# Kernel tuning notes

Hardware: AMD Instinct MI355X
Metric: run time of the kernel (lower is better)

The kernel has to match this reference:

```python
import jax, jax.numpy as jnp
import numpy as np

B, T = 64, 2048
DEC, ENC, ATT, LOC, K = 1024, 512, 128, 32, 31


def setup_inputs() -> dict:
    key = jax.random.key(0)
    ks = jax.random.split(key, 9)
    inv = lambda n: 1.0 / np.sqrt(n)
    return {
        "query": jax.random.normal(ks[0], (B, DEC), dtype=jnp.float32),
        "values": jax.random.normal(ks[1], (B, T, ENC), dtype=jnp.float32),
        "cumulative_attention_weights": jax.random.uniform(ks[2], (B, T), dtype=jnp.float32),
        "mask": jnp.zeros((B, T), dtype=bool),
        "Q_w": jax.random.uniform(ks[3], (ATT, DEC), jnp.float32, -inv(DEC), inv(DEC)),
        "Q_b": jax.random.uniform(ks[4], (ATT,), jnp.float32, -inv(DEC), inv(DEC)),
        "V_w": jax.random.uniform(ks[5], (ATT, ENC), jnp.float32, -inv(ENC), inv(ENC)),
        "conv_w": jax.random.uniform(ks[6], (LOC, 1, K), jnp.float32, -inv(K), inv(K)),
        "loc_proj_w": jax.random.uniform(ks[7], (ATT, LOC), jnp.float32, -inv(LOC), inv(LOC)),
        "v_w": jax.random.uniform(ks[8], (1, ATT), jnp.float32, -inv(ATT), inv(ATT)),
    }


def reference(query, values, cumulative_attention_weights, mask,
              Q_w, Q_b, V_w, conv_w, loc_proj_w, v_w):
    # query projection: [B, 1, ATT] (broadcast over T)
    q = query @ Q_w.T + Q_b                       # [B, ATT]
    q = q[:, None, :]
    # values cache: [B, T, ATT]
    v_cache = jnp.einsum("bte,ae->bta", values, V_w)
    # location features: Conv1d(1 -> LOC, k=31, same padding) over cum weights
    x = cumulative_attention_weights[:, None, :]   # [B, 1, T]
    loc = jax.lax.conv_general_dilated(
        x, conv_w, window_strides=(1,), padding="SAME",
        dimension_numbers=("NCH", "OIH", "NCH"))   # [B, LOC, T]
    loc = jnp.einsum("bct,ac->bta", loc, loc_proj_w)  # [B, T, ATT]
    # additive attention energies
    energies = jnp.tanh(q + v_cache + loc) @ v_w[0]   # [B, T]
    energies = jnp.where(mask, -jnp.inf, energies)
    attention_weights = jax.nn.softmax(energies, axis=1)
    # context: [B, ENC]
    attention_context = jnp.einsum("bt,bte->be", attention_weights, values)
    return attention_context, attention_weights
```

## Files before the change

kernel.cpp:

```cpp
#include <hip/hip_runtime.h>
#include <hip/hip_bf16.h>
#include <math.h>

#define B_  64
#define T_  2048
#define DEC_ 1024
#define ENC_ 512
#define ATT_ 128
#define LOC_ 32
#define KW_  31

typedef __attribute__((ext_vector_type(8))) short short8;
typedef __attribute__((ext_vector_type(4))) float f32x4;
typedef __attribute__((ext_vector_type(4))) unsigned int u32x4;

__device__ inline unsigned short bf16_rn(float x) {
    unsigned int u = __builtin_bit_cast(unsigned int, x);
    unsigned int r = u + 0x7fffu + ((u >> 16) & 1u);
    return (unsigned short)(r >> 16);
}
__device__ inline float bf16_to_f(unsigned short h) {
    unsigned int u = ((unsigned int)h) << 16;
    return __builtin_bit_cast(float, u);
}

__device__ inline void cvt_split8_exact(const float* f, short8& hi8, short8& lo8) {
    u32x4 hw, lw;
    #pragma unroll
    for (int p = 0; p < 4; ++p) {
        float a = f[2 * p], b2 = f[2 * p + 1];
        unsigned u0 = __builtin_bit_cast(unsigned, a);
        unsigned u1 = __builtin_bit_cast(unsigned, b2);
        unsigned r0 = u0 + 0x7fffu + ((u0 >> 16) & 1u);
        unsigned r1 = u1 + 0x7fffu + ((u1 >> 16) & 1u);
        hw[p] = (r0 >> 16) | (r1 & 0xffff0000u);
        float d0 = a  - __builtin_bit_cast(float, r0 & 0xffff0000u);
        float d1 = b2 - __builtin_bit_cast(float, r1 & 0xffff0000u);
        unsigned v0 = __builtin_bit_cast(unsigned, d0);
        unsigned v1 = __builtin_bit_cast(unsigned, d1);
        unsigned s0 = v0 + 0x7fffu + ((v0 >> 16) & 1u);
        unsigned s1 = v1 + 0x7fffu + ((v1 >> 16) & 1u);
        lw[p] = (s0 >> 16) | (s1 & 0xffff0000u);
    }
    hi8 = __builtin_bit_cast(short8, hw);
    lo8 = __builtin_bit_cast(short8, lw);
}

__global__ __launch_bounds__(256) void prep_kernel(
    const float* __restrict__ query, const float* __restrict__ Q_w,
    const float* __restrict__ Q_b, const float* __restrict__ conv_w,
    const float* __restrict__ loc_proj_w, const float* __restrict__ V_w,
    float* __restrict__ qbuf,
    unsigned short* __restrict__ Bph, unsigned short* __restrict__ Bpl,
    unsigned short* __restrict__ effh, unsigned short* __restrict__ effl)
{
    int bi = blockIdx.x, tid = threadIdx.x;
    if (bi < 256) {
        int b = bi >> 2, grp = bi & 3;
        __shared__ float sq[DEC_];
        *(float4*)(&sq[tid * 4]) = *(const float4*)(query + (size_t)b * DEC_ + tid * 4);
        __syncthreads();
        int w = tid >> 6, lane = tid & 63;
        int a0 = grp * 32 + w * 8;
        for (int p = 0; p < 4; ++p) {
            int a = a0 + 2 * p;
            const float* r0 = Q_w + (size_t)a * DEC_;
            const float* r1 = r0 + DEC_;
            float s0 = 0.f, s1 = 0.f;
            #pragma unroll
            for (int i = 0; i < 4; ++i) {
                float4 q0 = *(const float4*)(r0 + i * 256 + lane * 4);
                float4 q1 = *(const float4*)(r1 + i * 256 + lane * 4);
                float4 xq = *(const float4*)(sq + i * 256 + lane * 4);
                s0 += q0.x * xq.x + q0.y * xq.y + q0.z * xq.z + q0.w * xq.w;
                s1 += q1.x * xq.x + q1.y * xq.y + q1.z * xq.z + q1.w * xq.w;
            }
            #pragma unroll
            for (int m = 32; m >= 1; m >>= 1) {
                s0 += __shfl_xor(s0, m, 64);
                s1 += __shfl_xor(s1, m, 64);
            }
            if (lane == 0) {
                qbuf[b * ATT_ + a]     = s0 + Q_b[a];
                qbuf[b * ATT_ + a + 1] = s1 + Q_b[a + 1];
            }
        }
    } else if (bi == 256) {
        __shared__ float slp[ATT_ * LOC_];
        __shared__ float scw[LOC_ * KW_];
        for (int i = tid; i < ATT_ * LOC_; i += 256) slp[i] = loc_proj_w[i];
        for (int i = tid; i < LOC_ * KW_; i += 256) scw[i] = conv_w[i];
        __syncthreads();
        if (tid < ATT_) {
            int n = tid;
            for (int k = 0; k < 32; ++k) {
                float s = 0.f;
                if (k < KW_)
                    #pragma unroll
                    for (int c = 0; c < LOC_; ++c)
                        s += slp[n * LOC_ + c] * scw[c * KW_ + k];
                unsigned short h = bf16_rn(s);
                effh[n * 32 + k] = h;
                effl[n * 32 + k] = bf16_rn(s - bf16_to_f(h));
            }
        }
    } else {
        int g0 = (bi - 257) * 512;
        #pragma unroll
        for (int p = 0; p < 2; ++p) {
            int gi = g0 + p * 256 + tid;
            int n  = gi >> 7;
            int kq = (gi & 127) * 4;
            float4 v = ((const float4*)V_w)[gi];
            ushort4 h4, l4;
            h4.x = bf16_rn(v.x); l4.x = bf16_rn(v.x - bf16_to_f(h4.x));
            h4.y = bf16_rn(v.y); l4.y = bf16_rn(v.y - bf16_to_f(h4.y));
            h4.z = bf16_rn(v.z); l4.z = bf16_rn(v.z - bf16_to_f(h4.z));
            h4.w = bf16_rn(v.w); l4.w = bf16_rn(v.w - bf16_to_f(h4.w));
            int dst = (kq >> 5) * 4096 + n * 32 + (kq & 31);
            *(ushort4*)(Bph + dst) = h4;
            *(ushort4*)(Bpl + dst) = l4;
        }
    }
}

__global__ __launch_bounds__(256, 2) void energy_ctx_kernel(
    const float* __restrict__ values, const float* __restrict__ cum,
    const float* __restrict__ qbuf,
    const unsigned short* __restrict__ Bph, const unsigned short* __restrict__ Bpl,
    const unsigned short* __restrict__ effh, const unsigned short* __restrict__ effl,
    const float* __restrict__ vw, const unsigned char* __restrict__ mask,
    float* __restrict__ wU, float* __restrict__ bstats,
    float* __restrict__ ctxpart)
{
    __shared__ float sx[160];
    __shared__ float se[128];
    __shared__ float red[512];

    const int tid = threadIdx.x;
    const int bx  = blockIdx.x;
    const int b   = bx >> 4;
    const int t0  = (bx & 15) * 128;

    if (tid < 160) {
        int g = t0 - 15 + tid;
        sx[tid] = (g >= 0 && g < T_) ? cum[b * T_ + g] : 0.f;
    }
    __syncthreads();

    const int w      = tid >> 6;
    const int lane   = tid & 63;
    const int lane15 = lane & 15;
    const int quad   = lane >> 4;

    f32x4 acc[2][8];
    #pragma unroll
    for (int i = 0; i < 2; ++i)
        #pragma unroll
        for (int j = 0; j < 8; ++j) acc[i][j] = (f32x4){0.f, 0.f, 0.f, 0.f};

    const float* abase = values + ((size_t)b * T_ + t0 + w * 32 + lane15) * ENC_ + quad * 8;
    const unsigned short* bbh = Bph + lane15 * 32 + quad * 8;
    const unsigned short* bbl = Bpl + lane15 * 32 + quad * 8;

    float4 pfA[2][2], pfB[2][2];
    #pragma unroll
    for (int i = 0; i < 2; ++i) {
        pfA[i][0] = *(const float4*)(abase + i * 16 * ENC_);
        pfA[i][1] = *(const float4*)(abase + i * 16 * ENC_ + 4);
        pfB[i][0] = *(const float4*)(abase + i * 16 * ENC_ + 32);
        pfB[i][1] = *(const float4*)(abase + i * 16 * ENC_ + 36);
    }

    auto halfstep = [&](float4 (&pfX)[2][2], int kc, bool pre) {
        short8 ah[2], al[2];
        #pragma unroll
        for (int i = 0; i < 2; ++i) {
            float fb[8] = {pfX[i][0].x, pfX[i][0].y, pfX[i][0].z, pfX[i][0].w,
                           pfX[i][1].x, pfX[i][1].y, pfX[i][1].z, pfX[i][1].w};
            cvt_split8_exact(fb, ah[i], al[i]);
        }
        short8 bh[8], bl[8];
        const unsigned short* bb_h = bbh + (kc >> 5) * 4096;
        const unsigned short* bb_l = bbl + (kc >> 5) * 4096;
        #pragma unroll
        for (int j = 0; j < 8; ++j) {
            bh[j] = *(const short8*)(bb_h + j * 512);
            bl[j] = *(const short8*)(bb_l + j * 512);
        }
        __builtin_amdgcn_sched_barrier(0);
        if (pre) {
            #pragma unroll
            for (int i = 0; i < 2; ++i) {
                pfX[i][0] = *(const float4*)(abase + i * 16 * ENC_ + kc + 64);
                pfX[i][1] = *(const float4*)(abase + i * 16 * ENC_ + kc + 68);
            }
        }
        __builtin_amdgcn_sched_barrier(0);
        #pragma unroll
        for (int j = 0; j < 8; ++j)
            #pragma unroll
            for (int i = 0; i < 2; ++i) {
                acc[i][j] = __builtin_amdgcn_mfma_f32_16x16x32_bf16(ah[i], bh[j], acc[i][j], 0, 0, 0);
                acc[i][j] = __builtin_amdgcn_mfma_f32_16x16x32_bf16(ah[i], bl[j], acc[i][j], 0, 0, 0);
                acc[i][j] = __builtin_amdgcn_mfma_f32_16x16x32_bf16(al[i], bh[j], acc[i][j], 0, 0, 0);
            }
    };

    for (int kc = 0; kc < ENC_; kc += 64) {
        halfstep(pfA, kc,      kc + 64 < ENC_);
        halfstep(pfB, kc + 32, kc + 96 < ENC_);
    }

    {
        short8 ah[2], al[2];
        #pragma unroll
        for (int i = 0; i < 2; ++i) {
            int base = w * 32 + i * 16 + lane15 + quad * 8;
            float xv[8];
            #pragma unroll
            for (int j2 = 0; j2 < 8; ++j2) xv[j2] = sx[base + j2];
            cvt_split8_exact(xv, ah[i], al[i]);
        }
        #pragma unroll
        for (int j = 0; j < 8; ++j) {
            int n = j * 16 + lane15;
            short8 bh = *(const short8*)(effh + n * 32 + quad * 8);
            short8 bl = *(const short8*)(effl + n * 32 + quad * 8);
            #pragma unroll
            for (int i = 0; i < 2; ++i) {
                acc[i][j] = __builtin_amdgcn_mfma_f32_16x16x32_bf16(ah[i], bh, acc[i][j], 0, 0, 0);
                acc[i][j] = __builtin_amdgcn_mfma_f32_16x16x32_bf16(ah[i], bl, acc[i][j], 0, 0, 0);
                acc[i][j] = __builtin_amdgcn_mfma_f32_16x16x32_bf16(al[i], bh, acc[i][j], 0, 0, 0);
            }
        }
    }

    float qv[8], vv[8];
    #pragma unroll
    for (int j = 0; j < 8; ++j) {
        int n = j * 16 + lane15;
        qv[j] = qbuf[b * ATT_ + n];
        vv[j] = vw[n];
    }
    #pragma unroll
    for (int i = 0; i < 2; ++i)
        #pragma unroll
        for (int r = 0; r < 4; ++r) {
            float s = 0.f;
            #pragma unroll
            for (int j = 0; j < 8; ++j)
                s += vv[j] * tanhf(acc[i][j][r] + qv[j]);
            #pragma unroll
            for (int m = 8; m >= 1; m >>= 1) s += __shfl_xor(s, m, 64);
            if (lane15 == 0)
                se[w * 32 + i * 16 + quad * 4 + r] = s;
        }
    __syncthreads();

    if (tid < 128 && mask[b * T_ + t0 + tid]) se[tid] = -INFINITY;
    __syncthreads();

    float e0 = se[lane * 2], e1 = se[lane * 2 + 1];
    float mx = fmaxf(e0, e1);
    #pragma unroll
    for (int m = 32; m >= 1; m >>= 1) mx = fmaxf(mx, __shfl_xor(mx, m, 64));
    float w0 = 0.f, w1 = 0.f;
    if (mx > -INFINITY) {
        w0 = expf(e0 - mx);
        w1 = expf(e1 - mx);
    }
    float sm = w0 + w1;
    #pragma unroll
    for (int m = 32; m >= 1; m >>= 1) sm += __shfl_xor(sm, m, 64);
    __syncthreads();

    if (w == 0) {
        se[lane * 2]     = w0;
        se[lane * 2 + 1] = w1;
        *(float2*)(wU + b * T_ + t0 + lane * 2) = make_float2(w0, w1);
        if (lane == 0)
            *(float2*)(bstats + bx * 2) = make_float2(mx, sm);
    }
    __syncthreads();

    {
        int tt = tid >> 7;
        int e4 = (tid & 127) * 4;
        const float* vp = values + ((size_t)b * T_ + t0 + tt * 64) * ENC_ + e4;
        float4 cacc = make_float4(0.f, 0.f, 0.f, 0.f);
        #pragma unroll 8
        for (int t = 0; t < 64; ++t) {
            float4 v = *(const float4*)(vp + (size_t)t * ENC_);
            float wv = se[tt * 64 + t];
            cacc.x += wv * v.x; cacc.y += wv * v.y;
            cacc.z += wv * v.z; cacc.w += wv * v.w;
        }
        if (tt == 1) *(float4*)&red[e4] = cacc;
        __syncthreads();
        if (tt == 0) {
            float4 o = *(const float4*)&red[e4];
            float4 tot = make_float4(cacc.x + o.x, cacc.y + o.y,
                                     cacc.z + o.z, cacc.w + o.w);
            *(float4*)(ctxpart + (size_t)bx * ENC_ + e4) = tot;
        }
    }
}

__global__ __launch_bounds__(256) void combine_kernel(
    const float* __restrict__ bstats, const float* __restrict__ ctxpart,
    const float* __restrict__ wU, float* __restrict__ out)
{
    int b = blockIdx.x, tid = threadIdx.x;
    __shared__ float smx[16], ssm[16], ssc[16];
    if (tid < 16) {
        float2 st = *(const float2*)(bstats + (b * 16 + tid) * 2);
        smx[tid] = st.x; ssm[tid] = st.y;
    }
    __syncthreads();
    float M = -INFINITY;
    #pragma unroll
    for (int k = 0; k < 16; ++k) M = fmaxf(M, smx[k]);
    if (tid < 16)
        ssc[tid] = (smx[tid] > -INFINITY) ? expf(smx[tid] - M) : 0.f;
    __syncthreads();
    float S = 0.f;
    #pragma unroll
    for (int k = 0; k < 16; ++k) S += ssm[k] * ssc[k];
    float invS = 1.f / S;

    float* ctx  = out;
    float* wout = out + B_ * ENC_;

    float cx = 0.f, cy = 0.f;
    #pragma unroll
    for (int k = 0; k < 16; ++k) {
        float2 v = *(const float2*)(ctxpart + (size_t)(b * 16 + k) * ENC_ + tid * 2);
        cx += v.x * ssc[k]; cy += v.y * ssc[k];
    }
    *(float2*)(ctx + b * ENC_ + tid * 2) = make_float2(cx * invS, cy * invS);

    #pragma unroll
    for (int p = 0; p < 8; ++p) {
        int t = p * 256 + tid;
        wout[b * T_ + t] = wU[b * T_ + t] * ssc[t >> 7] * invS;
    }
}

extern "C" void kernel_launch(void* const* d_in, const int* in_sizes, int n_in,
                              void* d_out, int out_size, void* d_ws, size_t ws_size,
                              hipStream_t stream) {
    const float* query        = (const float*)d_in[0];
    const float* values       = (const float*)d_in[1];
    const float* cum          = (const float*)d_in[2];
    const unsigned char* mask = (const unsigned char*)d_in[3];
    const float* Q_w          = (const float*)d_in[4];
    const float* Q_b          = (const float*)d_in[5];
    const float* V_w          = (const float*)d_in[6];
    const float* conv_w       = (const float*)d_in[7];
    const float* loc_proj_w   = (const float*)d_in[8];
    const float* v_w          = (const float*)d_in[9];

    float* out = (float*)d_out;
    char*  ws  = (char*)d_ws;
    float*          qbuf     = (float*)(ws);
    unsigned short* Bph      = (unsigned short*)(ws + 32768);
    unsigned short* Bpl      = (unsigned short*)(ws + 163840);
    unsigned short* effh     = (unsigned short*)(ws + 294912);
    unsigned short* effl     = (unsigned short*)(ws + 303104);
    float*          wU       = (float*)(ws + 311296);
    float*          bstats   = (float*)(ws + 835584);
    float*          ctxpart  = (float*)(ws + 843776);

    prep_kernel<<<289, 256, 0, stream>>>(query, Q_w, Q_b, conv_w, loc_proj_w, V_w,
                                         qbuf, Bph, Bpl, effh, effl);
    energy_ctx_kernel<<<1024, 256, 0, stream>>>(values, cum, qbuf, Bph, Bpl,
                                                effh, effl, v_w, mask,
                                                wU, bstats, ctxpart);
    combine_kernel<<<B_, 256, 0, stream>>>(bstats, ctxpart, wU, out);
}
```

Before: 469.1 us.

## Stage packed V_w bf16 tiles into LDS via async global-to-LDS double buffering

Packs the hi/lo bf16 split of V_w into one interleaved buffer laid out per 32-wide K chunk. The energy kernel now double-buffers each chunk into shared memory with global_load_lds and block barriers, instead of every wave loading the B fragments directly from global or L2. The A-side prefetch drops from two halves to one chunk ahead. This adds 32KB of LDS per block, which may limit occupancy, and adds a barrier per K chunk.

```diff
diff --git a/kernel.cpp b/kernel.cpp
--- a/kernel.cpp
+++ b/kernel.cpp
@@ -50,8 +50,7 @@
     const float* __restrict__ query, const float* __restrict__ Q_w,
     const float* __restrict__ Q_b, const float* __restrict__ conv_w,
     const float* __restrict__ loc_proj_w, const float* __restrict__ V_w,
-    float* __restrict__ qbuf,
-    unsigned short* __restrict__ Bph, unsigned short* __restrict__ Bpl,
+    float* __restrict__ qbuf, unsigned short* __restrict__ Bpk,
     unsigned short* __restrict__ effh, unsigned short* __restrict__ effl)
 {
     int bi = blockIdx.x, tid = threadIdx.x;
@@ -117,22 +116,27 @@
             h4.y = bf16_rn(v.y); l4.y = bf16_rn(v.y - bf16_to_f(h4.y));
             h4.z = bf16_rn(v.z); l4.z = bf16_rn(v.z - bf16_to_f(h4.z));
             h4.w = bf16_rn(v.w); l4.w = bf16_rn(v.w - bf16_to_f(h4.w));
-            int dst = (kq >> 5) * 4096 + n * 32 + (kq & 31);
-            *(ushort4*)(Bph + dst) = h4;
-            *(ushort4*)(Bpl + dst) = l4;
+            int c = kq >> 5;
+            int j = n >> 7 == 0 ? (n >> 4) : (n >> 4);
+            int l = ((kq & 31) >> 3) * 16 + (n & 15);
+            int e = kq & 7;
+            int dst = c * 8192 + (n >> 4) * 512 + l * 8 + e;
+            (void)j;
+            *(ushort4*)(Bpk + dst)        = h4;
+            *(ushort4*)(Bpk + dst + 4096) = l4;
         }
     }
 }
 
 __global__ __launch_bounds__(256, 2) void energy_ctx_kernel(
     const float* __restrict__ values, const float* __restrict__ cum,
-    const float* __restrict__ qbuf,
-    const unsigned short* __restrict__ Bph, const unsigned short* __restrict__ Bpl,
+    const float* __restrict__ qbuf, const unsigned short* __restrict__ Bpk,
     const unsigned short* __restrict__ effh, const unsigned short* __restrict__ effl,
     const float* __restrict__ vw, const unsigned char* __restrict__ mask,
     float* __restrict__ wU, float* __restrict__ bstats,
     float* __restrict__ ctxpart)
 {
+    __shared__ unsigned short sB[2][8192];
     __shared__ float sx[160];
     __shared__ float se[128];
     __shared__ float red[512];
@@ -160,56 +164,71 @@
         for (int j = 0; j < 8; ++j) acc[i][j] = (f32x4){0.f, 0.f, 0.f, 0.f};
 
     const float* abase = values + ((size_t)b * T_ + t0 + w * 32 + lane15) * ENC_ + quad * 8;
-    const unsigned short* bbh = Bph + lane15 * 32 + quad * 8;
-    const unsigned short* bbl = Bpl + lane15 * 32 + quad * 8;
-
-    float4 pfA[2][2], pfB[2][2];
+
+    auto stageB = [&](int buf, int c) {
+        const unsigned short* src = Bpk + c * 8192 + w * 512 + lane * 8;
+        #pragma unroll
+        for (int r = 0; r < 4; ++r) {
+            __builtin_amdgcn_global_load_lds(
+                (const __attribute__((address_space(1))) unsigned int*)(src + r * 2048),
+                (__attribute__((address_space(3))) unsigned int*)(&sB[buf][r * 2048 + w * 512]),
+                16, 0, 0);
+        }
+    };
+
+    float4 pf[2][2];
+    stageB(0, 0);
+    __builtin_amdgcn_sched_barrier(0);
     #pragma unroll
     for (int i = 0; i < 2; ++i) {
-        pfA[i][0] = *(const float4*)(abase + i * 16 * ENC_);
-        pfA[i][1] = *(const float4*)(abase + i * 16 * ENC_ + 4);
-        pfB[i][0] = *(const float4*)(abase + i * 16 * ENC_ + 32);
-        pfB[i][1] = *(const float4*)(abase + i * 16 * ENC_ + 36);
-    }
-
-    auto halfstep = [&](float4 (&pfX)[2][2], int kc, bool pre) {
+        pf[i][0] = *(const float4*)(abase + i * 16 * ENC_);
+        pf[i][1] = *(const float4*)(abase + i * 16 * ENC_ + 4);
+    }
+    __builtin_amdgcn_sched_barrier(0);
+    asm volatile("s_waitcnt vmcnt(4)");
+    __builtin_amdgcn_sched_barrier(0);
+    __builtin_amdgcn_s_barrier();
+
+    int cur = 0;
+    for (int c = 0; c < 16; ++c) {
+        if (c + 1 < 16) stageB(cur ^ 1, c + 1);
+        __builtin_amdgcn_sched_barrier(0);
+
         short8 ah[2], al[2];
         #pragma unroll
         for (int i = 0; i < 2; ++i) {
-            float fb[8] = {pfX[i][0].x, pfX[i][0].y, pfX[i][0].z, pfX[i][0].w,
-                           pfX[i][1].x, pfX[i][1].y, pfX[i][1].z, pfX[i][1].w};
+            float fb[8] = {pf[i][0].x, pf[i][0].y, pf[i][0].z, pf[i][0].w,
+                           pf[i][1].x, pf[i][1].y, pf[i][1].z, pf[i][1].w};
             cvt_split8_exact(fb, ah[i], al[i]);
         }
-        short8 bh[8], bl[8];
-        const unsigned short* bb_h = bbh + (kc >> 5) * 4096;
-        const unsigned short* bb_l = bbl + (kc >> 5) * 4096;
+        if (c + 1 < 16) {
+            int kc = (c + 1) * 32;
+            #pragma unroll
+            for (int i = 0; i < 2; ++i) {
+                pf[i][0] = *(const float4*)(abase + i * 16 * ENC_ + kc);
+                pf[i][1] = *(const float4*)(abase + i * 16 * ENC_ + kc + 4);
+            }
+        }
+
         #pragma unroll
         for (int j = 0; j < 8; ++j) {
-            bh[j] = *(const short8*)(bb_h + j * 512);
-            bl[j] = *(const short8*)(bb_l + j * 512);
-        }
-        __builtin_amdgcn_sched_barrier(0);
-        if (pre) {
+            short8 bh = *(const short8*)&sB[cur][j * 512 + lane * 8];
+            short8 bl = *(const short8*)&sB[cur][4096 + j * 512 + lane * 8];
             #pragma unroll
             for (int i = 0; i < 2; ++i) {
-                pfX[i][0] = *(const float4*)(abase + i * 16 * ENC_ + kc + 64);
-                pfX[i][1] = *(const float4*)(abase + i * 16 * ENC_ + kc + 68);
-            }
-        }
-        __builtin_amdgcn_sched_barrier(0);
-        #pragma unroll
-        for (int j = 0; j < 8; ++j)
-            #pragma unroll
-            for (int i = 0; i < 2; ++i) {
-                acc[i][j] = __builtin_amdgcn_mfma_f32_16x16x32_bf16(ah[i], bh[j], acc[i][j], 0, 0, 0);
-                acc[i][j] = __builtin_amdgcn_mfma_f32_16x16x32_bf16(ah[i], bl[j], acc[i][j], 0, 0, 0);
-                acc[i][j] = __builtin_amdgcn_mfma_f32_16x16x32_bf16(al[i], bh[j], acc[i][j], 0, 0, 0);
-            }
-    };
-
-    for (int kc = 0; kc < ENC_; kc += 64) {
-        halfstep(pfA, kc,      kc + 64 < ENC_);
-        halfstep(pfB, kc + 32, kc + 96 < ENC_);
+                acc[i][j] = __builtin_amdgcn_mfma_f32_16x16x32_bf16(ah[i], bh, acc[i][j], 0, 0, 0);
+                acc[i][j] = __builtin_amdgcn_mfma_f32_16x16x32_bf16(ah[i], bl, acc[i][j], 0, 0, 0);
+                acc[i][j] = __builtin_amdgcn_mfma_f32_16x16x32_bf16(al[i], bh, acc[i][j], 0, 0, 0);
+            }
+        }
+
+        if (c + 1 < 16) {
+            __builtin_amdgcn_sched_barrier(0);
+            asm volatile("s_waitcnt vmcnt(4)");
+            __builtin_amdgcn_sched_barrier(0);
+            __builtin_amdgcn_s_barrier();
+            cur ^= 1;
+        }
     }
 
     {
@@ -364,8 +383,7 @@
     float* out = (float*)d_out;
     char*  ws  = (char*)d_ws;
     float*          qbuf     = (float*)(ws);
-    unsigned short* Bph      = (unsigned short*)(ws + 32768);
-    unsigned short* Bpl      = (unsigned short*)(ws + 163840);
+    unsigned short* Bpk      = (unsigned short*)(ws + 32768);
     unsigned short* effh     = (unsigned short*)(ws + 294912);
     unsigned short* effl     = (unsigned short*)(ws + 303104);
     float*          wU       = (float*)(ws + 311296);
@@ -373,8 +391,8 @@
     float*          ctxpart  = (float*)(ws + 843776);
 
     prep_kernel<<<289, 256, 0, stream>>>(query, Q_w, Q_b, conv_w, loc_proj_w, V_w,
-                                         qbuf, Bph, Bpl, effh, effl);
-    energy_ctx_kernel<<<1024, 256, 0, stream>>>(values, cum, qbuf, Bph, Bpl,
+                                         qbuf, Bpk, effh, effl);
+    energy_ctx_kernel<<<1024, 256, 0, stream>>>(values, cum, qbuf, Bpk,
                                                 effh, effl, v_w, mask,
                                                 wU, bstats, ctxpart);
     combine_kernel<<<B_, 256, 0, stream>>>(bstats, ctxpart, wU, out);
```

Result: no change. 460.3 us (-1.9%).

## Make energy/context work wave-local with 128-thread blocks and per-wave softmax partials

Applied to the files above, without the earlier changes.

Shrinks the energy kernel to 128-thread blocks of two independent waves. Each wave computes its own 32-timestep softmax partial and context partial, so block-wide barriers and the cross-wave shared reduction go away. The A-operand prefetch is simplified from two ping-pong buffers to one. The cost is four times as many partials (64 per batch) for the combine kernel to merge, and less prefetch depth to hide load latency.

```diff
diff --git a/kernel.cpp b/kernel.cpp
--- a/kernel.cpp
+++ b/kernel.cpp
@@ -124,7 +124,7 @@
     }
 }
 
-__global__ __launch_bounds__(256, 2) void energy_ctx_kernel(
+__global__ __launch_bounds__(128, 4) void energy_ctx_kernel(
     const float* __restrict__ values, const float* __restrict__ cum,
     const float* __restrict__ qbuf,
     const unsigned short* __restrict__ Bph, const unsigned short* __restrict__ Bpl,
@@ -133,67 +133,68 @@
     float* __restrict__ wU, float* __restrict__ bstats,
     float* __restrict__ ctxpart)
 {
-    __shared__ float sx[160];
-    __shared__ float se[128];
-    __shared__ float red[512];
-
-    const int tid = threadIdx.x;
-    const int bx  = blockIdx.x;
-    const int b   = bx >> 4;
-    const int t0  = (bx & 15) * 128;
-
-    if (tid < 160) {
-        int g = t0 - 15 + tid;
-        sx[tid] = (g >= 0 && g < T_) ? cum[b * T_ + g] : 0.f;
-    }
-    __syncthreads();
-
-    const int w      = tid >> 6;
-    const int lane   = tid & 63;
+    __shared__ float sxw[2][80];
+    __shared__ float sew[2][32];
+
+    const int tid  = threadIdx.x;
+    const int bx   = blockIdx.x;
+    const int b    = bx >> 5;
+    const int sub  = bx & 31;
+    const int w    = tid >> 6;
+    const int lane = tid & 63;
+    const int t0w  = sub * 64 + w * 32;
+    const int cid  = sub * 2 + w;
+
     const int lane15 = lane & 15;
     const int quad   = lane >> 4;
 
+    {
+        int g = t0w - 15 + lane;
+        sxw[w][lane] = (g >= 0 && g < T_) ? cum[b * T_ + g] : 0.f;
+        if (lane < 16) {
+            int g2 = t0w + 49 + lane;
+            sxw[w][64 + lane] = (g2 >= 0 && g2 < T_) ? cum[b * T_ + g2] : 0.f;
+        }
+    }
+
     f32x4 acc[2][8];
     #pragma unroll
     for (int i = 0; i < 2; ++i)
         #pragma unroll
         for (int j = 0; j < 8; ++j) acc[i][j] = (f32x4){0.f, 0.f, 0.f, 0.f};
 
-    const float* abase = values + ((size_t)b * T_ + t0 + w * 32 + lane15) * ENC_ + quad * 8;
+    const float* abase = values + ((size_t)b * T_ + t0w + lane15) * ENC_ + quad * 8;
     const unsigned short* bbh = Bph + lane15 * 32 + quad * 8;
     const unsigned short* bbl = Bpl + lane15 * 32 + quad * 8;
 
-    float4 pfA[2][2], pfB[2][2];
+    float4 pf[2][2];
     #pragma unroll
     for (int i = 0; i < 2; ++i) {
-        pfA[i][0] = *(const float4*)(abase + i * 16 * ENC_);
-        pfA[i][1] = *(const float4*)(abase + i * 16 * ENC_ + 4);
-        pfB[i][0] = *(const float4*)(abase + i * 16 * ENC_ + 32);
-        pfB[i][1] = *(const float4*)(abase + i * 16 * ENC_ + 36);
-    }
-
-    auto halfstep = [&](float4 (&pfX)[2][2], int kc, bool pre) {
+        pf[i][0] = *(const float4*)(abase + i * 16 * ENC_);
+        pf[i][1] = *(const float4*)(abase + i * 16 * ENC_ + 4);
+    }
+
+    for (int kc = 0; kc < ENC_; kc += 32) {
         short8 ah[2], al[2];
         #pragma unroll
         for (int i = 0; i < 2; ++i) {
-            float fb[8] = {pfX[i][0].x, pfX[i][0].y, pfX[i][0].z, pfX[i][0].w,
-                           pfX[i][1].x, pfX[i][1].y, pfX[i][1].z, pfX[i][1].w};
+            float fb[8] = {pf[i][0].x, pf[i][0].y, pf[i][0].z, pf[i][0].w,
+                           pf[i][1].x, pf[i][1].y, pf[i][1].z, pf[i][1].w};
             cvt_split8_exact(fb, ah[i], al[i]);
         }
         short8 bh[8], bl[8];
-        const unsigned short* bb_h = bbh + (kc >> 5) * 4096;
-        const unsigned short* bb_l = bbl + (kc >> 5) * 4096;
+        const int chunk = (kc >> 5) * 4096;
         #pragma unroll
         for (int j = 0; j < 8; ++j) {
-            bh[j] = *(const short8*)(bb_h + j * 512);
-            bl[j] = *(const short8*)(bb_l + j * 512);
+            bh[j] = *(const short8*)(bbh + chunk + j * 512);
+            bl[j] = *(const short8*)(bbl + chunk + j * 512);
         }
         __builtin_amdgcn_sched_barrier(0);
-        if (pre) {
+        if (kc + 32 < ENC_) {
             #pragma unroll
             for (int i = 0; i < 2; ++i) {
-                pfX[i][0] = *(const float4*)(abase + i * 16 * ENC_ + kc + 64);
-                pfX[i][1] = *(const float4*)(abase + i * 16 * ENC_ + kc + 68);
+                pf[i][0] = *(const float4*)(abase + i * 16 * ENC_ + kc + 32);
+                pf[i][1] = *(const float4*)(abase + i * 16 * ENC_ + kc + 36);
             }
         }
         __builtin_amdgcn_sched_barrier(0);
@@ -205,21 +206,16 @@
                 acc[i][j] = __builtin_amdgcn_mfma_f32_16x16x32_bf16(ah[i], bl[j], acc[i][j], 0, 0, 0);
                 acc[i][j] = __builtin_amdgcn_mfma_f32_16x16x32_bf16(al[i], bh[j], acc[i][j], 0, 0, 0);
             }
-    };
-
-    for (int kc = 0; kc < ENC_; kc += 64) {
-        halfstep(pfA, kc,      kc + 64 < ENC_);
-        halfstep(pfB, kc + 32, kc + 96 < ENC_);
     }
 
     {
         short8 ah[2], al[2];
         #pragma unroll
         for (int i = 0; i < 2; ++i) {
-            int base = w * 32 + i * 16 + lane15 + quad * 8;
+            int base = i * 16 + lane15 + quad * 8;
             float xv[8];
             #pragma unroll
-            for (int j2 = 0; j2 < 8; ++j2) xv[j2] = sx[base + j2];
+            for (int j2 = 0; j2 < 8; ++j2) xv[j2] = sxw[w][base + j2];
             cvt_split8_exact(xv, ah[i], al[i]);
         }
         #pragma unroll
@@ -254,56 +250,45 @@
             #pragma unroll
             for (int m = 8; m >= 1; m >>= 1) s += __shfl_xor(s, m, 64);
             if (lane15 == 0)
-                se[w * 32 + i * 16 + quad * 4 + r] = s;
-        }
-    __syncthreads();
-
-    if (tid < 128 && mask[b * T_ + t0 + tid]) se[tid] = -INFINITY;
-    __syncthreads();
-
-    float e0 = se[lane * 2], e1 = se[lane * 2 + 1];
-    float mx = fmaxf(e0, e1);
+                sew[w][i * 16 + quad * 4 + r] = s;
+        }
+
+    float e = (lane < 32) ? sew[w][lane] : -INFINITY;
+    if (lane < 32 && mask[b * T_ + t0w + lane]) e = -INFINITY;
+    float mx = e;
     #pragma unroll
     for (int m = 32; m >= 1; m >>= 1) mx = fmaxf(mx, __shfl_xor(mx, m, 64));
-    float w0 = 0.f, w1 = 0.f;
-    if (mx > -INFINITY) {
-        w0 = expf(e0 - mx);
-        w1 = expf(e1 - mx);
-    }
-    float sm = w0 + w1;
+    float w0 = 0.f;
+    if (mx > -INFINITY && lane < 32) w0 = expf(e - mx);
+    float sm = w0;
     #pragma unroll
     for (int m = 32; m >= 1; m >>= 1) sm += __shfl_xor(sm, m, 64);
-    __syncthreads();
-
-    if (w == 0) {
-        se[lane * 2]     = w0;
-        se[lane * 2 + 1] = w1;
-        *(float2*)(wU + b * T_ + t0 + lane * 2) = make_float2(w0, w1);
-        if (lane == 0)
-            *(float2*)(bstats + bx * 2) = make_float2(mx, sm);
-    }
-    __syncthreads();
+
+    if (lane < 32) {
+        sew[w][lane] = w0;
+        wU[b * T_ + t0w + lane] = w0;
+    }
+    if (lane == 0)
+        *(float2*)(bstats + (b * 64 + cid) * 2) = make_float2(mx, sm);
 
     {
-        int tt = tid >> 7;
-        int e4 = (tid & 127) * 4;
-        const float* vp = values + ((size_t)b * T_ + t0 + tt * 64) * ENC_ + e4;
-        float4 cacc = make_float4(0.f, 0.f, 0.f, 0.f);
+        int e8 = lane * 8;
+        const float* vp = values + ((size_t)b * T_ + t0w) * ENC_ + e8;
+        float4 c0 = make_float4(0.f, 0.f, 0.f, 0.f);
+        float4 c1 = make_float4(0.f, 0.f, 0.f, 0.f);
         #pragma unroll 8
-        for (int t = 0; t < 64; ++t) {
-            float4 v = *(const float4*)(vp + (size_t)t * ENC_);
-            float wv = se[tt * 64 + t];
-            cacc.x += wv * v.x; cacc.y += wv * v.y;
-            cacc.z += wv * v.z; cacc.w += wv * v.w;
-        }
-        if (tt == 1) *(float4*)&red[e4] = cacc;
-        __syncthreads();
-        if (tt == 0) {
-            float4 o = *(const float4*)&red[e4];
-            float4 tot = make_float4(cacc.x + o.x, cacc.y + o.y,
-                                     cacc.z + o.z, cacc.w + o.w);
-            *(float4*)(ctxpart + (size_t)bx * ENC_ + e4) = tot;
-        }
+        for (int t = 0; t < 32; ++t) {
+            float4 v0 = *(const float4*)(vp + (size_t)t * ENC_);
+            float4 v1 = *(const float4*)(vp + (size_t)t * ENC_ + 4);
+            float wv = sew[w][t];
+            c0.x += wv * v0.x; c0.y += wv * v0.y;
+            c0.z += wv * v0.z; c0.w += wv * v0.w;
+            c1.x += wv * v1.x; c1.y += wv * v1.y;
+            c1.z += wv * v1.z; c1.w += wv * v1.w;
+        }
+        float* cp = ctxpart + (size_t)(b * 64 + cid) * ENC_ + e8;
+        *(float4*)(cp)     = c0;
+        *(float4*)(cp + 4) = c1;
     }
 }
 
@@ -312,30 +297,30 @@
     const float* __restrict__ wU, float* __restrict__ out)
 {
     int b = blockIdx.x, tid = threadIdx.x;
-    __shared__ float smx[16], ssm[16], ssc[16];
-    if (tid < 16) {
-        float2 st = *(const float2*)(bstats + (b * 16 + tid) * 2);
+    __shared__ float smx[64], ssm[64], ssc[64];
+    if (tid < 64) {
+        float2 st = *(const float2*)(bstats + (b * 64 + tid) * 2);
         smx[tid] = st.x; ssm[tid] = st.y;
     }
     __syncthreads();
     float M = -INFINITY;
     #pragma unroll
-    for (int k = 0; k < 16; ++k) M = fmaxf(M, smx[k]);
-    if (tid < 16)
+    for (int k = 0; k < 64; ++k) M = fmaxf(M, smx[k]);
+    if (tid < 64)
         ssc[tid] = (smx[tid] > -INFINITY) ? expf(smx[tid] - M) : 0.f;
     __syncthreads();
     float S = 0.f;
     #pragma unroll
-    for (int k = 0; k < 16; ++k) S += ssm[k] * ssc[k];
+    for (int k = 0; k < 64; ++k) S += ssm[k] * ssc[k];
     float invS = 1.f / S;
 
     float* ctx  = out;
     float* wout = out + B_ * ENC_;
 
     float cx = 0.f, cy = 0.f;
-    #pragma unroll
-    for (int k = 0; k < 16; ++k) {
-        float2 v = *(const float2*)(ctxpart + (size_t)(b * 16 + k) * ENC_ + tid * 2);
+    #pragma unroll 8
+    for (int k = 0; k < 64; ++k) {
+        float2 v = *(const float2*)(ctxpart + (size_t)(b * 64 + k) * ENC_ + tid * 2);
         cx += v.x * ssc[k]; cy += v.y * ssc[k];
     }
     *(float2*)(ctx + b * ENC_ + tid * 2) = make_float2(cx * invS, cy * invS);
@@ -343,7 +328,7 @@
     #pragma unroll
     for (int p = 0; p < 8; ++p) {
         int t = p * 256 + tid;
-        wout[b * T_ + t] = wU[b * T_ + t] * ssc[t >> 7] * invS;
+        wout[b * T_ + t] = wU[b * T_ + t] * ssc[t >> 5] * invS;
     }
 }
 
@@ -370,11 +355,11 @@
     unsigned short* effl     = (unsigned short*)(ws + 303104);
     float*          wU       = (float*)(ws + 311296);
     float*          bstats   = (float*)(ws + 835584);
-    float*          ctxpart  = (float*)(ws + 843776);
+    float*          ctxpart  = (float*)(ws + 868352);
 
     prep_kernel<<<289, 256, 0, stream>>>(query, Q_w, Q_b, conv_w, loc_proj_w, V_w,
                                          qbuf, Bph, Bpl, effh, effl);
-    energy_ctx_kernel<<<1024, 256, 0, stream>>>(values, cum, qbuf, Bph, Bpl,
+    energy_ctx_kernel<<<2048, 128, 0, stream>>>(values, cum, qbuf, Bph, Bpl,
                                                 effh, effl, v_w, mask,
                                                 wU, bstats, ctxpart);
     combine_kernel<<<B_, 256, 0, stream>>>(bstats, ctxpart, wU, out);
```

Result: slower. 770.5 us (+64.3%).

## Split energy GEMM over 8 waves with LDS-staged bf16 split of values

Applied to the files above, without the earlier changes.

Raises the energy/context block to 512 threads and arranges the 8 waves as a 4x2 grid over rows and attention columns. Each wave converts one 16x32 slab of values to hi/lo bf16 once and stages it in double-buffered LDS, with a barrier per K-chunk. The partial energies from the two column halves are summed through shared memory. The intent is more waves per CU and less register pressure to hide global-load latency, at the cost of per-chunk block barriers and extra LDS traffic.

```diff
diff --git a/kernel.cpp b/kernel.cpp
--- a/kernel.cpp
+++ b/kernel.cpp
@@ -23,7 +23,6 @@
     unsigned int u = ((unsigned int)h) << 16;
     return __builtin_bit_cast(float, u);
 }
-
 __device__ inline void cvt_split8_exact(const float* f, short8& hi8, short8& lo8) {
     u32x4 hw, lw;
     #pragma unroll
@@ -124,7 +123,7 @@
     }
 }
 
-__global__ __launch_bounds__(256, 2) void energy_ctx_kernel(
+__global__ __launch_bounds__(512, 4) void energy_ctx_kernel(
     const float* __restrict__ values, const float* __restrict__ cum,
     const float* __restrict__ qbuf,
     const unsigned short* __restrict__ Bph, const unsigned short* __restrict__ Bpl,
@@ -133,7 +132,10 @@
     float* __restrict__ wU, float* __restrict__ bstats,
     float* __restrict__ ctxpart)
 {
+    __shared__ unsigned short sAh[2][4096];
+    __shared__ unsigned short sAl[2][4096];
     __shared__ float sx[160];
+    __shared__ float sep[2][128];
     __shared__ float se[128];
     __shared__ float red[512];
 
@@ -146,85 +148,108 @@
         int g = t0 - 15 + tid;
         sx[tid] = (g >= 0 && g < T_) ? cum[b * T_ + g] : 0.f;
     }
-    __syncthreads();
 
     const int w      = tid >> 6;
     const int lane   = tid & 63;
     const int lane15 = lane & 15;
     const int quad   = lane >> 4;
-
-    f32x4 acc[2][8];
+    const int wr     = w >> 1;
+    const int wc     = w & 1;
+
+    f32x4 acc[2][4];
     #pragma unroll
     for (int i = 0; i < 2; ++i)
         #pragma unroll
-        for (int j = 0; j < 8; ++j) acc[i][j] = (f32x4){0.f, 0.f, 0.f, 0.f};
-
-    const float* abase = values + ((size_t)b * T_ + t0 + w * 32 + lane15) * ENC_ + quad * 8;
-    const unsigned short* bbh = Bph + lane15 * 32 + quad * 8;
-    const unsigned short* bbl = Bpl + lane15 * 32 + quad * 8;
-
-    float4 pfA[2][2], pfB[2][2];
-    #pragma unroll
-    for (int i = 0; i < 2; ++i) {
-        pfA[i][0] = *(const float4*)(abase + i * 16 * ENC_);
-        pfA[i][1] = *(const float4*)(abase + i * 16 * ENC_ + 4);
-        pfB[i][0] = *(const float4*)(abase + i * 16 * ENC_ + 32);
-        pfB[i][1] = *(const float4*)(abase + i * 16 * ENC_ + 36);
-    }
-
-    auto halfstep = [&](float4 (&pfX)[2][2], int kc, bool pre) {
+        for (int j = 0; j < 4; ++j) acc[i][j] = (f32x4){0.f, 0.f, 0.f, 0.f};
+
+    const float* wsrc = values + ((size_t)b * T_ + t0 + w * 16 + lane15) * ENC_ + quad * 8;
+    const unsigned short* bbh = Bph + wc * 2048 + lane15 * 32 + quad * 8;
+    const unsigned short* bbl = Bpl + wc * 2048 + lane15 * 32 + quad * 8;
+
+    float4 pA[2][2];
+    pA[0][0] = *(const float4*)(wsrc);
+    pA[0][1] = *(const float4*)(wsrc + 4);
+    pA[1][0] = *(const float4*)(wsrc + 32);
+    pA[1][1] = *(const float4*)(wsrc + 36);
+
+    {
+        float fb[8] = {pA[0][0].x, pA[0][0].y, pA[0][0].z, pA[0][0].w,
+                       pA[0][1].x, pA[0][1].y, pA[0][1].z, pA[0][1].w};
+        short8 h8, l8;
+        cvt_split8_exact(fb, h8, l8);
+        *(short8*)&sAh[0][(w * 64 + lane) * 8] = h8;
+        *(short8*)&sAl[0][(w * 64 + lane) * 8] = l8;
+    }
+    __syncthreads();
+
+    #pragma unroll
+    for (int c = 0; c < 16; ++c) {
+        const int cur = c & 1;
+        if (c + 2 < 16) {
+            pA[cur][0] = *(const float4*)(wsrc + (c + 2) * 32);
+            pA[cur][1] = *(const float4*)(wsrc + (c + 2) * 32 + 4);
+        }
+        __builtin_amdgcn_sched_barrier(0);
+
         short8 ah[2], al[2];
         #pragma unroll
         for (int i = 0; i < 2; ++i) {
-            float fb[8] = {pfX[i][0].x, pfX[i][0].y, pfX[i][0].z, pfX[i][0].w,
-                           pfX[i][1].x, pfX[i][1].y, pfX[i][1].z, pfX[i][1].w};
-            cvt_split8_exact(fb, ah[i], al[i]);
-        }
-        short8 bh[8], bl[8];
-        const unsigned short* bb_h = bbh + (kc >> 5) * 4096;
-        const unsigned short* bb_l = bbl + (kc >> 5) * 4096;
-        #pragma unroll
-        for (int j = 0; j < 8; ++j) {
-            bh[j] = *(const short8*)(bb_h + j * 512);
-            bl[j] = *(const short8*)(bb_l + j * 512);
-        }
-        __builtin_amdgcn_sched_barrier(0);
-        if (pre) {
-            #pragma unroll
-            for (int i = 0; i < 2; ++i) {
-                pfX[i][0] = *(const float4*)(abase + i * 16 * ENC_ + kc + 64);
-                pfX[i][1] = *(const float4*)(abase + i * 16 * ENC_ + kc + 68);
-            }
-        }
-        __builtin_amdgcn_sched_barrier(0);
-        #pragma unroll
-        for (int j = 0; j < 8; ++j)
-            #pragma unroll
-            for (int i = 0; i < 2; ++i) {
-                acc[i][j] = __builtin_amdgcn_mfma_f32_16x16x32_bf16(ah[i], bh[j], acc[i][j], 0, 0, 0);
-                acc[i][j] = __builtin_amdgcn_mfma_f32_16x16x32_bf16(ah[i], bl[j], acc[i][j], 0, 0, 0);
-                acc[i][j] = __builtin_amdgcn_mfma_f32_16x16x32_bf16(al[i], bh[j], acc[i][j], 0, 0, 0);
-            }
-    };
-
-    for (int kc = 0; kc < ENC_; kc += 64) {
-        halfstep(pfA, kc,      kc + 64 < ENC_);
-        halfstep(pfB, kc + 32, kc + 96 < ENC_);
+            ah[i] = *(const short8*)&sAh[cur][((wr * 2 + i) * 64 + lane) * 8];
+            al[i] = *(const short8*)&sAl[cur][((wr * 2 + i) * 64 + lane) * 8];
+        }
+
+        if (c + 1 < 16) {
+            float fb[8] = {pA[cur ^ 1][0].x, pA[cur ^ 1][0].y,
+                           pA[cur ^ 1][0].z, pA[cur ^ 1][0].w,
+                           pA[cur ^ 1][1].x, pA[cur ^ 1][1].y,
+                           pA[cur ^ 1][1].z, pA[cur ^ 1][1].w};
+            short8 h8, l8;
+            cvt_split8_exact(fb, h8, l8);
+            *(short8*)&sAh[cur ^ 1][(w * 64 + lane) * 8] = h8;
+            *(short8*)&sAl[cur ^ 1][(w * 64 + lane) * 8] = l8;
+        }
+
+        const int chunk = (c >> 0) * 0 + (c * 0);
+        const int coff  = (c) * 4096;
+        #pragma unroll
+        for (int jp = 0; jp < 2; ++jp) {
+            short8 bh[2], bl[2];
+            #pragma unroll
+            for (int u = 0; u < 2; ++u) {
+                bh[u] = *(const short8*)(bbh + coff + (jp * 2 + u) * 512);
+                bl[u] = *(const short8*)(bbl + coff + (jp * 2 + u) * 512);
+            }
+            #pragma unroll
+            for (int u = 0; u < 2; ++u)
+                #pragma unroll
+                for (int i = 0; i < 2; ++i) {
+                    acc[i][jp * 2 + u] = __builtin_amdgcn_mfma_f32_16x16x32_bf16(ah[i], bh[u], acc[i][jp * 2 + u], 0, 0, 0);
+                    acc[i][jp * 2 + u] = __builtin_amdgcn_mfma_f32_16x16x32_bf16(ah[i], bl[u], acc[i][jp * 2 + u], 0, 0, 0);
+                    acc[i][jp * 2 + u] = __builtin_amdgcn_mfma_f32_16x16x32_bf16(al[i], bh[u], acc[i][jp * 2 + u], 0, 0, 0);
+                }
+        }
+
+        if (c + 1 < 16) {
+            __builtin_amdgcn_sched_barrier(0);
+            asm volatile("s_waitcnt lgkmcnt(0)" ::: "memory");
+            __builtin_amdgcn_s_barrier();
+        }
+        (void)chunk;
     }
 
     {
         short8 ah[2], al[2];
         #pragma unroll
         for (int i = 0; i < 2; ++i) {
-            int base = w * 32 + i * 16 + lane15 + quad * 8;
+            int base = wr * 32 + i * 16 + lane15 + quad * 8;
             float xv[8];
             #pragma unroll
             for (int j2 = 0; j2 < 8; ++j2) xv[j2] = sx[base + j2];
             cvt_split8_exact(xv, ah[i], al[i]);
         }
         #pragma unroll
-        for (int j = 0; j < 8; ++j) {
-            int n = j * 16 + lane15;
+        for (int j = 0; j < 4; ++j) {
+            int n = wc * 64 + j * 16 + lane15;
             short8 bh = *(const short8*)(effh + n * 32 + quad * 8);
             short8 bl = *(const short8*)(effl + n * 32 + quad * 8);
             #pragma unroll
@@ -236,10 +261,10 @@
         }
     }
 
-    float qv[8], vv[8];
-    #pragma unroll
-    for (int j = 0; j < 8; ++j) {
-        int n = j * 16 + lane15;
+    float qv[4], vv[4];
+    #pragma unroll
+    for (int j = 0; j < 4; ++j) {
+        int n = wc * 64 + j * 16 + lane15;
         qv[j] = qbuf[b * ATT_ + n];
         vv[j] = vw[n];
     }
@@ -249,16 +274,20 @@
         for (int r = 0; r < 4; ++r) {
             float s = 0.f;
             #pragma unroll
-            for (int j = 0; j < 8; ++j)
+            for (int j = 0; j < 4; ++j)
                 s += vv[j] * tanhf(acc[i][j][r] + qv[j]);
             #pragma unroll
             for (int m = 8; m >= 1; m >>= 1) s += __shfl_xor(s, m, 64);
             if (lane15 == 0)
-                se[w * 32 + i * 16 + quad * 4 + r] = s;
-        }
-    __syncthreads();
-
-    if (tid < 128 && mask[b * T_ + t0 + tid]) se[tid] = -INFINITY;
+                sep[wc][wr * 32 + i * 16 + quad * 4 + r] = s;
+        }
+    __syncthreads();
+
+    if (tid < 128) {
+        float ee = sep[0][tid] + sep[1][tid];
+        if (mask[b * T_ + t0 + tid]) ee = -INFINITY;
+        se[tid] = ee;
+    }
     __syncthreads();
 
     float e0 = se[lane * 2], e1 = se[lane * 2 + 1];
@@ -285,24 +314,22 @@
     __syncthreads();
 
     {
-        int tt = tid >> 7;
-        int e4 = (tid & 127) * 4;
-        const float* vp = values + ((size_t)b * T_ + t0 + tt * 64) * ENC_ + e4;
-        float4 cacc = make_float4(0.f, 0.f, 0.f, 0.f);
+        int tt = tid >> 8;
+        int e2 = (tid & 255) * 2;
+        const float* vp = values + ((size_t)b * T_ + t0 + tt * 64) * ENC_ + e2;
+        float cx = 0.f, cy = 0.f;
         #pragma unroll 8
         for (int t = 0; t < 64; ++t) {
-            float4 v = *(const float4*)(vp + (size_t)t * ENC_);
+            float2 v = *(const float2*)(vp + (size_t)t * ENC_);
             float wv = se[tt * 64 + t];
-            cacc.x += wv * v.x; cacc.y += wv * v.y;
-            cacc.z += wv * v.z; cacc.w += wv * v.w;
-        }
-        if (tt == 1) *(float4*)&red[e4] = cacc;
+            cx += wv * v.x; cy += wv * v.y;
+        }
+        if (tt == 1) *(float2*)&red[e2] = make_float2(cx, cy);
         __syncthreads();
         if (tt == 0) {
-            float4 o = *(const float4*)&red[e4];
-            float4 tot = make_float4(cacc.x + o.x, cacc.y + o.y,
-                                     cacc.z + o.z, cacc.w + o.w);
-            *(float4*)(ctxpart + (size_t)bx * ENC_ + e4) = tot;
+            float2 o = *(const float2*)&red[e2];
+            *(float2*)(ctxpart + (size_t)bx * ENC_ + e2) =
+                make_float2(cx + o.x, cy + o.y);
         }
     }
 }
@@ -374,7 +401,7 @@
 
     prep_kernel<<<289, 256, 0, stream>>>(query, Q_w, Q_b, conv_w, loc_proj_w, V_w,
                                          qbuf, Bph, Bpl, effh, effl);
-    energy_ctx_kernel<<<1024, 256, 0, stream>>>(values, cum, qbuf, Bph, Bpl,
+    energy_ctx_kernel<<<1024, 512, 0, stream>>>(values, cum, qbuf, Bph, Bpl,
                                                 effh, effl, v_w, mask,
                                                 wU, bstats, ctxpart);
     combine_kernel<<<B_, 256, 0, stream>>>(bstats, ctxpart, wU, out);
```

Result: no change. 461.7 us (-1.6%).
